# Kernel optimization log

Measured on AMD Instinct MI355X. Metric: run time of the kernel, lower is better.

## Reference

```python
import jax, jax.numpy as jnp
import numpy as np

N = 30000
E = 600000
IN = 64
HID = 128
EPS = 1e-5
HEADS_PER_LAYER = (4, 4, 1)


def _bn(x, g, b):
    # eval-mode BatchNorm: running_mean=0, running_var=1
    return x * (g / np.sqrt(1.0 + EPS)) + b


def _segment_softmax(e, dst, n):
    m = jax.ops.segment_max(e, dst, num_segments=n)
    ex = jnp.exp(e - m[dst])
    s = jax.ops.segment_sum(ex, dst, num_segments=n)
    return ex / (s[dst] + 1e-16)


def _gcn_conv(x, w, b, src, dst, norm, n):
    m = (x @ w)[src] * norm[:, None]            # [E+N, HID]
    return jax.ops.segment_sum(m, dst, num_segments=n) + b


def _gat_conv(x, w, a_src, a_dst, b, src, dst, n, heads):
    C = HID // heads
    xh = (x @ w).reshape(n, heads, C)
    asrc = (xh * a_src.reshape(heads, C)).sum(-1)   # [N, heads]
    adst = (xh * a_dst.reshape(heads, C)).sum(-1)
    e = jax.nn.leaky_relu(asrc[src] + adst[dst], 0.2)  # [E+N, heads]
    alpha = _segment_softmax(e, dst, n)
    out = jax.ops.segment_sum(xh[src] * alpha[:, :, None], dst, num_segments=n)
    return out.reshape(n, HID) + b


def _forward(x, gcn_in_w, gcn_in_b, gcn_res_w, gcn_res_b, gcn_w, gcn_b,
             gcn_bn_g, gcn_bn_b, gcn_c1w, gcn_c1b, gcn_c2w, gcn_c2b,
             gcn_c3w, gcn_c3b, gat_in_w, gat_in_b, gat_w, gat_asrc,
             gat_adst, gat_b, gat_bn_g, gat_bn_b, feat_imp, gat_c1w,
             gat_c1b, gat_cbn_g, gat_cbn_b, gat_c2w, gat_c2b, gat_c3w,
             gat_c3b, fin_w, fin_b, fin_bn_g, fin_bn_b, fin2_w, fin2_b,
             edge_index):
    n = x.shape[0]
    loop = jnp.arange(n, dtype=edge_index.dtype)
    src = jnp.concatenate([edge_index[0], loop])  # add self-loops
    dst = jnp.concatenate([edge_index[1], loop])
    # GCN symmetric normalization (with self-loops)
    deg = jax.ops.segment_sum(jnp.ones_like(dst, dtype=x.dtype), dst, num_segments=n)
    dis = jnp.where(deg > 0, jax.lax.rsqrt(jnp.maximum(deg, 1.0)), 0.0)
    norm = dis[src] * dis[dst]

    # ---- GCN branch (eval: dropout = identity, self-attn skipped since N>5000) ----
    xp = x @ gcn_in_w + gcn_in_b
    res = x @ gcn_res_w + gcn_res_b
    for i in range(3):
        xn = _gcn_conv(xp, gcn_w[i], gcn_b[i], src, dst, norm, n)
        xn = jax.nn.relu(_bn(xn, gcn_bn_g[i], gcn_bn_b[i]))
        if i % 2 == 1:
            xp = xn + res
            res = xp
        else:
            xp = xn
    h = jax.nn.relu(xp @ gcn_c1w + gcn_c1b)
    h = jax.nn.relu(h @ gcn_c2w + gcn_c2b)
    gcn_out = h @ gcn_c3w + gcn_c3b

    # ---- GAT branch ----
    xg = x @ gat_in_w + gat_in_b
    for i in range(3):
        xg = _gat_conv(xg, gat_w[i], gat_asrc[i], gat_adst[i], gat_b[i],
                       src, dst, n, HEADS_PER_LAYER[i])
        xg = jax.nn.elu(_bn(xg, gat_bn_g[i], gat_bn_b[i]))
    xg = xg * feat_imp
    h = jax.nn.relu(xg @ gat_c1w + gat_c1b)
    h = _bn(h, gat_cbn_g, gat_cbn_b)
    h = jax.nn.relu(h @ gat_c2w + gat_c2b)
    gat_out = h @ gat_c3w + gat_c3b

    # ---- fusion: N > 10000 -> weighted blend path ----
    fused = 0.6 * gcn_out + 0.4 * gat_out
    h = jax.nn.relu(fused @ fin_w + fin_b)
    h = _bn(h, fin_bn_g, fin_bn_b)
    return h @ fin2_w + fin2_b  # [N, 2]


def setup_inputs() -> dict:
    key = jax.random.key(0)
    ks = iter(jax.random.split(key, 64))

    def nrm(shape, scale=1.0):
        return jax.random.normal(next(ks), shape, dtype=jnp.float32) * scale

    s_in = 1.0 / np.sqrt(IN)
    s_h = 1.0 / np.sqrt(HID)
    inp = {}
    inp['x'] = nrm((N, IN))
    inp['edge_index'] = jax.random.randint(next(ks), (2, E), 0, N, dtype=jnp.int32)
    inp['gcn_in_w'] = nrm((IN, HID), s_in); inp['gcn_in_b'] = nrm((HID,), 0.01)
    inp['gcn_res_w'] = nrm((IN, HID), s_in); inp['gcn_res_b'] = nrm((HID,), 0.01)
    inp['gcn_w'] = nrm((3, HID, HID), s_h); inp['gcn_b'] = nrm((3, HID), 0.01)
    inp['gcn_bn_g'] = 1.0 + nrm((3, HID), 0.1); inp['gcn_bn_b'] = nrm((3, HID), 0.1)
    inp['gcn_c1w'] = nrm((HID, 64), s_h); inp['gcn_c1b'] = nrm((64,), 0.01)
    inp['gcn_c2w'] = nrm((64, 32), 0.125); inp['gcn_c2b'] = nrm((32,), 0.01)
    inp['gcn_c3w'] = nrm((32, HID), 0.18); inp['gcn_c3b'] = nrm((HID,), 0.01)
    inp['gat_in_w'] = nrm((IN, HID), s_in); inp['gat_in_b'] = nrm((HID,), 0.01)
    inp['gat_w'] = nrm((3, HID, HID), s_h)
    inp['gat_asrc'] = nrm((3, HID), s_h); inp['gat_adst'] = nrm((3, HID), s_h)
    inp['gat_b'] = nrm((3, HID), 0.01)
    inp['gat_bn_g'] = 1.0 + nrm((3, HID), 0.1); inp['gat_bn_b'] = nrm((3, HID), 0.1)
    inp['feat_imp'] = 1.0 + nrm((HID,), 0.1)
    inp['gat_c1w'] = nrm((HID, 64), s_h); inp['gat_c1b'] = nrm((64,), 0.01)
    inp['gat_cbn_g'] = 1.0 + nrm((64,), 0.1); inp['gat_cbn_b'] = nrm((64,), 0.1)
    inp['gat_c2w'] = nrm((64, 32), 0.125); inp['gat_c2b'] = nrm((32,), 0.01)
    inp['gat_c3w'] = nrm((32, HID), 0.18); inp['gat_c3b'] = nrm((HID,), 0.01)
    inp['fin_w'] = nrm((HID, 64), s_h); inp['fin_b'] = nrm((64,), 0.01)
    inp['fin_bn_g'] = 1.0 + nrm((64,), 0.1); inp['fin_bn_b'] = nrm((64,), 0.1)
    inp['fin2_w'] = nrm((64, 2), 0.125); inp['fin2_b'] = nrm((2,), 0.01)
    return inp


def reference(x, edge_index, gcn_in_w, gcn_in_b, gcn_res_w, gcn_res_b, gcn_w,
              gcn_b, gcn_bn_g, gcn_bn_b, gcn_c1w, gcn_c1b, gcn_c2w, gcn_c2b,
              gcn_c3w, gcn_c3b, gat_in_w, gat_in_b, gat_w, gat_asrc, gat_adst,
              gat_b, gat_bn_g, gat_bn_b, feat_imp, gat_c1w, gat_c1b, gat_cbn_g,
              gat_cbn_b, gat_c2w, gat_c2b, gat_c3w, gat_c3b, fin_w, fin_b,
              fin_bn_g, fin_bn_b, fin2_w, fin2_b):
    return _forward(x, gcn_in_w, gcn_in_b, gcn_res_w, gcn_res_b, gcn_w, gcn_b,
                    gcn_bn_g, gcn_bn_b, gcn_c1w, gcn_c1b, gcn_c2w, gcn_c2b,
                    gcn_c3w, gcn_c3b, gat_in_w, gat_in_b, gat_w, gat_asrc,
                    gat_adst, gat_b, gat_bn_g, gat_bn_b, feat_imp, gat_c1w,
                    gat_c1b, gat_cbn_g, gat_cbn_b, gat_c2w, gat_c2b, gat_c3w,
                    gat_c3b, fin_w, fin_b, fin_bn_g, fin_bn_b, fin2_w, fin2_b,
                    edge_index)
```

## Files before the change

kernel.cpp:

```cpp
#include <hip/hip_runtime.h>
#include <hip/hip_fp16.h>

#define RSQ_BN 0.9999950000374997f

typedef _Float16 f16x8 __attribute__((ext_vector_type(8)));
typedef float f32x4 __attribute__((ext_vector_type(4)));

__device__ __forceinline__ float leaky02(float x) { return x > 0.f ? x : 0.2f * x; }

__device__ __forceinline__ float4 ld4(const float* p) {
    return *reinterpret_cast<const float4*>(p);
}
__device__ __forceinline__ void st4(float* p, float4 v) {
    *reinterpret_cast<float4*>(p) = v;
}
__device__ __forceinline__ float4 h4f(uint2 u) {
    union { uint2 u; __half2 h[2]; } pk;
    pk.u = u;
    float2 lo = __half22float2(pk.h[0]);
    float2 hi = __half22float2(pk.h[1]);
    return make_float4(lo.x, lo.y, hi.x, hi.y);
}
__device__ __forceinline__ float4 f4z() { return make_float4(0.f, 0.f, 0.f, 0.f); }
__device__ __forceinline__ float4 f4bias(float4 v, float4 b) {
    return make_float4(v.x + b.x, v.y + b.y, v.z + b.z, v.w + b.w);
}
__device__ __forceinline__ float4 f4relu(float4 v) {
    return make_float4(fmaxf(v.x, 0.f), fmaxf(v.y, 0.f), fmaxf(v.z, 0.f), fmaxf(v.w, 0.f));
}
__device__ __forceinline__ float4 f4bn(float4 v, float4 g, float4 b) {
    return make_float4(v.x * g.x + b.x, v.y * g.y + b.y, v.z * g.z + b.z, v.w * g.w + b.w);
}
__device__ __forceinline__ float4 f4s(float4 v, float s) {
    return make_float4(v.x * s, v.y * s, v.z * s, v.w * s);
}


__global__ void zero_i32_k(int* __restrict__ p, int n) {
    int i = blockIdx.x * 256 + threadIdx.x;
    if (i < n) p[i] = 0;
}

__global__ void hist_k(const int* __restrict__ edst, int* __restrict__ cnt, int E, int EN) {
    int i = blockIdx.x * 256 + threadIdx.x;
    if (i >= EN) return;
    int d = (i < E) ? edst[i] : (i - E);
    atomicAdd(&cnt[d], 1);
}

__global__ __launch_bounds__(256)
void scanA_k(const int* __restrict__ cnt, int* __restrict__ rowptr,
             int* __restrict__ bsum, int n) {
    __shared__ int sh[256];
    int t = threadIdx.x;
    int i = blockIdx.x * 256 + t;
    int v = (i < n) ? cnt[i] : 0;
    sh[t] = v;
    __syncthreads();
#pragma unroll
    for (int off = 1; off < 256; off <<= 1) {
        int u = 0;
        if (t >= off) u = sh[t - off];
        __syncthreads();
        sh[t] += u;
        __syncthreads();
    }
    if (i < n) rowptr[i] = sh[t] - v;
    if (t == 255) bsum[blockIdx.x] = sh[255];
}

__global__ __launch_bounds__(256)
void scanB_k(int* __restrict__ bsum, int nb) {
    __shared__ int sh[256];
    int t = threadIdx.x;
    int v = (t < nb) ? bsum[t] : 0;
    sh[t] = v;
    __syncthreads();
#pragma unroll
    for (int off = 1; off < 256; off <<= 1) {
        int u = 0;
        if (t >= off) u = sh[t - off];
        __syncthreads();
        sh[t] += u;
        __syncthreads();
    }
    if (t < nb) bsum[t] = sh[t] - v;
}

__global__ __launch_bounds__(256)
void scanC_k(const int* __restrict__ cnt, const int* __restrict__ bsum,
             int* __restrict__ rowptr, int* __restrict__ cursor,
             float* __restrict__ dis, int n, int EN) {
    int i = blockIdx.x * 256 + threadIdx.x;
    if (i < n) {
        int r = rowptr[i] + bsum[blockIdx.x];
        rowptr[i] = r;
        cursor[i] = r;
        dis[i] = rsqrtf((float)cnt[i]);
    }
    if (i == 0) rowptr[n] = EN;
}

__global__ void scatter_k(const int* __restrict__ esrc, const int* __restrict__ edst,
                          int* __restrict__ cursor, int* __restrict__ colidx, int E, int EN) {
    int i = blockIdx.x * 256 + threadIdx.x;
    if (i >= EN) return;
    int s, d;
    if (i < E) { s = esrc[i]; d = edst[i]; }
    else       { s = i - E; d = s; }
    int pos = atomicAdd(&cursor[d], 1);
    colidx[pos] = s;
}


__global__ void wtx_all_k(const float* __restrict__ gcn_in_w, const float* __restrict__ gcn_res_w,
                          const float* __restrict__ gat_in_w,
                          const float* __restrict__ gcn_w, const float* __restrict__ gat_w,
                          const float* __restrict__ gcn_c1w, const float* __restrict__ gat_c1w,
                          const float* __restrict__ gcn_c3w, const float* __restrict__ gat_c3w,
                          const float* __restrict__ fin_w,
                          __half* __restrict__ WTin, __half* __restrict__ WTg,
                          __half* __restrict__ WTa, __half* __restrict__ WTc1,
                          __half* __restrict__ WTc3, __half* __restrict__ WTfin) {
    int idx = blockIdx.x * 256 + threadIdx.x;
    const float* src;
    __half* dst;
    int K, M, o;
    if (idx < 24576) {
        int mi = idx >> 13; o = idx & 8191;
        src = mi == 0 ? gcn_in_w : (mi == 1 ? gcn_res_w : gat_in_w);
        dst = WTin + mi * 8192; K = 64; M = 128;
    } else if (idx < 73728) {
        int r = idx - 24576; int mi = r >> 14; o = r & 16383;
        src = gcn_w + mi * 16384; dst = WTg + mi * 16384; K = 128; M = 128;
    } else if (idx < 122880) {
        int r = idx - 73728; int mi = r >> 14; o = r & 16383;
        src = gat_w + mi * 16384; dst = WTa + mi * 16384; K = 128; M = 128;
    } else if (idx < 139264) {
        int r = idx - 122880; int mi = r >> 13; o = r & 8191;
        src = mi ? gat_c1w : gcn_c1w; dst = WTc1 + mi * 8192; K = 128; M = 64;
    } else if (idx < 147456) {
        int r = idx - 139264; int mi = r >> 12; o = r & 4095;
        src = mi ? gat_c3w : gcn_c3w; dst = WTc3 + mi * 4096; K = 32; M = 128;
    } else if (idx < 155648) {
        o = idx - 147456; src = fin_w; dst = WTfin; K = 128; M = 64;
    } else return;
    int mcol = o / K, k = o - mcol * K;
    dst[o] = (__half)src[k * M + mcol];
}


#define FMA4R(A_, xv, w0, w1, w2, w3)                                  \
    A_.x += xv.x * w0.x + xv.y * w1.x + xv.z * w2.x + xv.w * w3.x;     \
    A_.y += xv.x * w0.y + xv.y * w1.y + xv.z * w2.y + xv.w * w3.y;     \
    A_.z += xv.x * w0.z + xv.y * w1.z + xv.z * w2.z + xv.w * w3.z;     \
    A_.w += xv.x * w0.w + xv.y * w1.w + xv.z * w2.w + xv.w * w3.w;

template <int K, int M>
__device__ __forceinline__ void gemm4(const float* __restrict__ Ws,
                                      const float* xa, const float* xb,
                                      const float* xc, const float* xd, int c,
                                      float4& A, float4& B, float4& C, float4& D) {
#pragma unroll 4
    for (int k = 0; k < K; k += 4) {
        float4 va = ld4(xa + k), vb = ld4(xb + k), vc = ld4(xc + k), vd = ld4(xd + k);
        const float* wp = Ws + k * M + c;
        float4 w0 = ld4(wp), w1 = ld4(wp + M), w2 = ld4(wp + 2 * M), w3 = ld4(wp + 3 * M);
        FMA4R(A, va, w0, w1, w2, w3)
        FMA4R(B, vb, w0, w1, w2, w3)
        FMA4R(C, vc, w0, w1, w2, w3)
        FMA4R(D, vd, w0, w1, w2, w3)
    }
}

template <int K, int M>
__global__ __launch_bounds__(256)
void tail2_k(const float* __restrict__ X0, const float* __restrict__ W0, const float* __restrict__ b0,
             float* __restrict__ Y0,
             const float* __restrict__ X1, const float* __restrict__ W1, const float* __restrict__ b1,
             float* __restrict__ Y1,
             int n, int gper, int do_relu) {
    constexpr int CG = M / 4, RPB = 256 / CG;
    bool s1 = blockIdx.x >= gper;
    int blk = s1 ? blockIdx.x - gper : blockIdx.x;
    const float* X = s1 ? X1 : X0;
    const float* W = s1 ? W1 : W0;
    const float* bi = s1 ? b1 : b0;
    float* Y = s1 ? Y1 : Y0;
    __shared__ float Ws[K * M];
    for (int i = threadIdx.x; i < K * M; i += 256) Ws[i] = W[i];
    __syncthreads();
    int cg = threadIdx.x % CG, r = threadIdx.x / CG, c = cg * 4;
    int ra = blk * (4 * RPB) + r, rb = ra + RPB, rc = ra + 2 * RPB, rd = ra + 3 * RPB;
    const float* xa = X + (size_t)(ra < n ? ra : 0) * K;
    const float* xb = X + (size_t)(rb < n ? rb : 0) * K;
    const float* xc = X + (size_t)(rc < n ? rc : 0) * K;
    const float* xd = X + (size_t)(rd < n ? rd : 0) * K;
    float4 A = f4z(), B = f4z(), C = f4z(), D = f4z();
    gemm4<K, M>(Ws, xa, xb, xc, xd, c, A, B, C, D);
    float4 bv = ld4(bi + c);
    A = f4bias(A, bv); B = f4bias(B, bv); C = f4bias(C, bv); D = f4bias(D, bv);
    if (do_relu) { A = f4relu(A); B = f4relu(B); C = f4relu(C); D = f4relu(D); }
    if (ra < n) st4(Y + (size_t)ra * M + c, A);
    if (rb < n) st4(Y + (size_t)rb * M + c, B);
    if (rc < n) st4(Y + (size_t)rc * M + c, C);
    if (rd < n) st4(Y + (size_t)rd * M + c, D);
}


__device__ __forceinline__ f16x8 mk_af(const float* xr, int kb) {
    float4 v0 = ld4(xr + kb), v1 = ld4(xr + kb + 4);
    f16x8 af;
    af[0] = (_Float16)v0.x; af[1] = (_Float16)v0.y;
    af[2] = (_Float16)v0.z; af[3] = (_Float16)v0.w;
    af[4] = (_Float16)v1.x; af[5] = (_Float16)v1.y;
    af[6] = (_Float16)v1.z; af[7] = (_Float16)v1.w;
    return af;
}

__global__ __launch_bounds__(256)
void mfma_lin3_k(const float* __restrict__ X, const __half* __restrict__ WTin,
                 const float* __restrict__ b0, float* __restrict__ Y0,
                 const float* __restrict__ b1, float* __restrict__ Y1,
                 const float* __restrict__ b2, float* __restrict__ Y2,
                 int n, int gper) {
    constexpr int K = 64, CT = 8;
    int set = blockIdx.x / gper, blk = blockIdx.x % gper;
    const __half* WT = WTin + (size_t)set * 8192;
    const float* bi = set == 0 ? b0 : (set == 1 ? b1 : b2);
    float* Y = set == 0 ? Y0 : (set == 1 ? Y1 : Y2);
    int wave = threadIdx.x >> 6, lane = threadIdx.x & 63;
    int m = lane & 15, quad = lane >> 4;
    int row0 = blk * 64 + wave * 16;
    int arow = min(row0 + m, n - 1);
    const float* xr = X + (size_t)arow * K;
    f32x4 acc[CT];
#pragma unroll
    for (int ct = 0; ct < CT; ++ct) acc[ct] = (f32x4){0.f, 0.f, 0.f, 0.f};
#pragma unroll
    for (int k32 = 0; k32 < K / 32; ++k32) {
        int kb = k32 * 32 + quad * 8;
        f16x8 af = mk_af(xr, kb);
#pragma unroll
        for (int ct = 0; ct < CT; ++ct) {
            f16x8 bf = *reinterpret_cast<const f16x8*>(WT + (size_t)(ct * 16 + m) * K + kb);
            acc[ct] = __builtin_amdgcn_mfma_f32_16x16x32_f16(af, bf, acc[ct], 0, 0, 0);
        }
    }
#pragma unroll
    for (int ct = 0; ct < CT; ++ct) {
        int col = ct * 16 + m;
        float cb = bi[col];
#pragma unroll
        for (int reg = 0; reg < 4; ++reg) {
            int row = row0 + quad * 4 + reg;
            if (row < n) Y[(size_t)row * 128 + col] = acc[ct][reg] + cb;
        }
    }
}

template <int K, int M>
__global__ __launch_bounds__(256)
void mfma_lin2_k(const float* __restrict__ X0, const __half* __restrict__ WT0,
                 const float* __restrict__ b0, const float* __restrict__ g0,
                 const float* __restrict__ bb0, float* __restrict__ Y0,
                 const float* __restrict__ X1, const __half* __restrict__ WT1,
                 const float* __restrict__ b1, const float* __restrict__ g1,
                 const float* __restrict__ bb1, float* __restrict__ Y1,
                 int n, int gper, int do_relu) {
    constexpr int CT = M / 16;
    bool s1 = blockIdx.x >= gper;
    int blk = s1 ? blockIdx.x - gper : blockIdx.x;
    const float* X = s1 ? X1 : X0;
    const __half* WT = s1 ? WT1 : WT0;
    const float* bi = s1 ? b1 : b0;
    const float* bg = s1 ? g1 : g0;
    const float* bb = s1 ? bb1 : bb0;
    float* Y = s1 ? Y1 : Y0;
    int wave = threadIdx.x >> 6, lane = threadIdx.x & 63;
    int m = lane & 15, quad = lane >> 4;
    int row0 = blk * 64 + wave * 16;
    int arow = min(row0 + m, n - 1);
    const float* xr = X + (size_t)arow * K;
    f32x4 acc[CT];
#pragma unroll
    for (int ct = 0; ct < CT; ++ct) acc[ct] = (f32x4){0.f, 0.f, 0.f, 0.f};
#pragma unroll
    for (int k32 = 0; k32 < K / 32; ++k32) {
        int kb = k32 * 32 + quad * 8;
        f16x8 af = mk_af(xr, kb);
#pragma unroll
        for (int ct = 0; ct < CT; ++ct) {
            f16x8 bf = *reinterpret_cast<const f16x8*>(WT + (size_t)(ct * 16 + m) * K + kb);
            acc[ct] = __builtin_amdgcn_mfma_f32_16x16x32_f16(af, bf, acc[ct], 0, 0, 0);
        }
    }
#pragma unroll
    for (int ct = 0; ct < CT; ++ct) {
        int col = ct * 16 + m;
        float cb = bi[col];
        float cg = bg ? bg[col] * RSQ_BN : 1.f;
        float cbb = bg ? bb[col] : 0.f;
#pragma unroll
        for (int reg = 0; reg < 4; ++reg) {
            int row = row0 + quad * 4 + reg;
            if (row < n) {
                float v = acc[ct][reg] + cb;
                if (do_relu) v = fmaxf(v, 0.f);
                if (bg) v = v * cg + cbb;
                Y[(size_t)row * M + col] = v;
            }
        }
    }
}

__global__ __launch_bounds__(256)
void mfma_linF_k(const float* __restrict__ XA, const float* __restrict__ XB,
                 const __half* __restrict__ WT, const float* __restrict__ bi,
                 const float* __restrict__ bg, const float* __restrict__ bb,
                 const float* __restrict__ w2, const float* __restrict__ b2,
                 float* __restrict__ out, int n) {
    constexpr int K = 128, M = 64, CT = 4;
    int wave = threadIdx.x >> 6, lane = threadIdx.x & 63;
    int m = lane & 15, quad = lane >> 4;
    int row0 = blockIdx.x * 64 + wave * 16;
    int arow = min(row0 + m, n - 1);
    const float* xra = XA + (size_t)arow * K;
    const float* xrb = XB + (size_t)arow * K;
    f32x4 acc[CT];
#pragma unroll
    for (int ct = 0; ct < CT; ++ct) acc[ct] = (f32x4){0.f, 0.f, 0.f, 0.f};
#pragma unroll
    for (int k32 = 0; k32 < K / 32; ++k32) {
        int kb = k32 * 32 + quad * 8;
        float4 a0 = ld4(xra + kb), a1 = ld4(xra + kb + 4);
        float4 u0 = ld4(xrb + kb), u1 = ld4(xrb + kb + 4);
        f16x8 af;
        af[0] = (_Float16)(0.6f * a0.x + 0.4f * u0.x);
        af[1] = (_Float16)(0.6f * a0.y + 0.4f * u0.y);
        af[2] = (_Float16)(0.6f * a0.z + 0.4f * u0.z);
        af[3] = (_Float16)(0.6f * a0.w + 0.4f * u0.w);
        af[4] = (_Float16)(0.6f * a1.x + 0.4f * u1.x);
        af[5] = (_Float16)(0.6f * a1.y + 0.4f * u1.y);
        af[6] = (_Float16)(0.6f * a1.z + 0.4f * u1.z);
        af[7] = (_Float16)(0.6f * a1.w + 0.4f * u1.w);
#pragma unroll
        for (int ct = 0; ct < CT; ++ct) {
            f16x8 bf = *reinterpret_cast<const f16x8*>(WT + (size_t)(ct * 16 + m) * K + kb);
            acc[ct] = __builtin_amdgcn_mfma_f32_16x16x32_f16(af, bf, acc[ct], 0, 0, 0);
        }
    }
    float p0[4] = {0.f, 0.f, 0.f, 0.f}, p1[4] = {0.f, 0.f, 0.f, 0.f};
#pragma unroll
    for (int ct = 0; ct < CT; ++ct) {
        int col = ct * 16 + m;
        float cb = bi[col];
        float cg = bg[col] * RSQ_BN;
        float cbb = bb[col];
        float w20 = w2[2 * col], w21 = w2[2 * col + 1];
#pragma unroll
        for (int reg = 0; reg < 4; ++reg) {
            float v = fmaxf(acc[ct][reg] + cb, 0.f) * cg + cbb;
            p0[reg] += v * w20;
            p1[reg] += v * w21;
        }
    }
    for (int off = 1; off < 16; off <<= 1) {
#pragma unroll
        for (int reg = 0; reg < 4; ++reg) {
            p0[reg] += __shfl_xor(p0[reg], off);
            p1[reg] += __shfl_xor(p1[reg], off);
        }
    }
    if (m == 0) {
#pragma unroll
        for (int reg = 0; reg < 4; ++reg) {
            int row = row0 + quad * 4 + reg;
            if (row < n) {
                out[row * 2] = p0[reg] + b2[0];
                out[row * 2 + 1] = p1[reg] + b2[1];
            }
        }
    }
}


__global__ __launch_bounds__(256)
void dual128_mfma_k(const float* __restrict__ Xg, const __half* __restrict__ WTg,
                    __half* __restrict__ Yg,
                    const float* __restrict__ Xa, const __half* __restrict__ WTa,
                    __half* __restrict__ Ya,
                    const float* __restrict__ dis,
                    const float* __restrict__ asrc, const float* __restrict__ adst,
                    float* __restrict__ avp, float* __restrict__ bvp,
                    int hh, int n, int gper) {
    bool gat = blockIdx.x >= gper;
    int blk = gat ? blockIdx.x - gper : blockIdx.x;
    const float* X = gat ? Xa : Xg;
    const __half* WT = gat ? WTa : WTg;
    __half* Y = gat ? Ya : Yg;
    int wave = threadIdx.x >> 6;
    int lane = threadIdx.x & 63;
    int m = lane & 15, quad = lane >> 4;
    int row0 = blk * 64 + wave * 16;
    int arow = min(row0 + m, n - 1);
    const float* xr = X + (size_t)arow * 128;
    f32x4 acc[8];
#pragma unroll
    for (int ct = 0; ct < 8; ++ct) acc[ct] = (f32x4){0.f, 0.f, 0.f, 0.f};
#pragma unroll
    for (int k32 = 0; k32 < 4; ++k32) {
        int kb = k32 * 32 + quad * 8;
        f16x8 af = mk_af(xr, kb);
#pragma unroll
        for (int ct = 0; ct < 8; ++ct) {
            f16x8 bf = *reinterpret_cast<const f16x8*>(WT + (size_t)(ct * 16 + m) * 128 + kb);
            acc[ct] = __builtin_amdgcn_mfma_f32_16x16x32_f16(af, bf, acc[ct], 0, 0, 0);
        }
    }
    if (!gat) {
#pragma unroll
        for (int reg = 0; reg < 4; ++reg) {
            int row = row0 + quad * 4 + reg;
            if (row < n) {
                float dv = dis[row];
#pragma unroll
                for (int ct = 0; ct < 8; ++ct)
                    Y[(size_t)row * 128 + ct * 16 + m] = (__half)(acc[ct][reg] * dv);
            }
        }
    } else {
        float cas[8], cad[8];
#pragma unroll
        for (int ct = 0; ct < 8; ++ct) {
            cas[ct] = asrc[ct * 16 + m];
            cad[ct] = adst[ct * 16 + m];
        }
        int ctph = 8 / hh;
#pragma unroll
        for (int reg = 0; reg < 4; ++reg) {
            int row = row0 + quad * 4 + reg;
            bool valid = row < n;
            if (valid) {
#pragma unroll
                for (int ct = 0; ct < 8; ++ct)
                    Y[(size_t)row * 128 + ct * 16 + m] = (__half)acc[ct][reg];
            }
            for (int h = 0; h < hh; ++h) {
                float sa = 0.f, sd = 0.f;
                for (int j = 0; j < ctph; ++j) {
                    int ct = h * ctph + j;
                    sa += acc[ct][reg] * cas[ct];
                    sd += acc[ct][reg] * cad[ct];
                }
                for (int off = 1; off < 16; off <<= 1) {
                    sa += __shfl_xor(sa, off);
                    sd += __shfl_xor(sd, off);
                }
                if (m == 0 && valid) {
                    avp[row * hh + h] = sa;
                    bvp[row * hh + h] = sd;
                }
            }
        }
    }
}


__global__ __launch_bounds__(256)
void fused_gather_k(const int* __restrict__ rowptr, const int* __restrict__ colidx,
                    const float* __restrict__ dis,
                    const __half* __restrict__ Tg, const float* __restrict__ gbias,
                    const float* __restrict__ gbng, const float* __restrict__ gbnb,
                    const float* __restrict__ res, float* __restrict__ Yg,
                    const __half* __restrict__ Ta, const float* __restrict__ avp,
                    const float* __restrict__ bvp, const float* __restrict__ abias,
                    const float* __restrict__ abng, const float* __restrict__ abnb,
                    const float* __restrict__ fimp, float* __restrict__ Ya,
                    int n, int hh, int log2C) {
    int idx = blockIdx.x * 256 + threadIdx.x;
    int i = idx >> 4;
    if (i >= n) return;
    int c = (idx & 15) * 8;
    int h = c >> log2C;
    float ad = bvp[i * hh + h];
    int p0 = rowptr[i], p1 = rowptr[i + 1];
    float4 glo = f4z(), ghi = f4z();
    float4 alo = f4z(), ahi = f4z();
    float m = -3.0e38f, s = 0.f;

#define GACC(qq)                                                                \
    {                                                                           \
        float4 t0 = h4f(make_uint2(qq.x, qq.y)), t1 = h4f(make_uint2(qq.z, qq.w)); \
        glo.x += t0.x; glo.y += t0.y; glo.z += t0.z; glo.w += t0.w;             \
        ghi.x += t1.x; ghi.y += t1.y; ghi.z += t1.z; ghi.w += t1.w;             \
    }
#define AACC(qq, ww)                                                            \
    {                                                                           \
        float4 t0 = h4f(make_uint2(qq.x, qq.y)), t1 = h4f(make_uint2(qq.z, qq.w)); \
        alo.x += t0.x * ww; alo.y += t0.y * ww; alo.z += t0.z * ww; alo.w += t0.w * ww; \
        ahi.x += t1.x * ww; ahi.y += t1.y * ww; ahi.z += t1.z * ww; ahi.w += t1.w * ww; \
    }

    int p = p0;
    int nfull = (p1 - p0) >> 2;
    int sx[4];
    if (nfull > 0) {
#pragma unroll
        for (int j = 0; j < 4; ++j) sx[j] = colidx[p + j];
    }
    for (int g = 0; g < nfull; ++g) {
        float e[4]; uint4 qg[4], qa[4];
#pragma unroll
        for (int j = 0; j < 4; ++j) e[j] = leaky02(avp[sx[j] * hh + h] + ad);
#pragma unroll
        for (int j = 0; j < 4; ++j)
            qg[j] = *reinterpret_cast<const uint4*>(Tg + (size_t)sx[j] * 128 + c);
#pragma unroll
        for (int j = 0; j < 4; ++j)
            qa[j] = *reinterpret_cast<const uint4*>(Ta + (size_t)sx[j] * 128 + c);
        int sn[4];
        int pn = p + 4;
        bool more = (g + 1) < nfull;
#pragma unroll
        for (int j = 0; j < 4; ++j) sn[j] = more ? colidx[pn + j] : 0;
#pragma unroll
        for (int j = 0; j < 4; ++j) GACC(qg[j])
        float mc = fmaxf(fmaxf(e[0], e[1]), fmaxf(e[2], e[3]));
        float mn = fmaxf(m, mc);
        float scale = expf(m - mn);
        alo = f4s(alo, scale);
        ahi = f4s(ahi, scale);
        float wsum = 0.f;
#pragma unroll
        for (int j = 0; j < 4; ++j) {
            float wj = expf(e[j] - mn);
            wsum += wj;
            AACC(qa[j], wj)
        }
        s = s * scale + wsum;
        m = mn;
        p = pn;
#pragma unroll
        for (int j = 0; j < 4; ++j) sx[j] = sn[j];
    }
    for (; p < p1; ++p) {
        int s0 = colidx[p];
        float e0 = leaky02(avp[s0 * hh + h] + ad);
        uint4 qg0 = *reinterpret_cast<const uint4*>(Tg + (size_t)s0 * 128 + c);
        uint4 qa0 = *reinterpret_cast<const uint4*>(Ta + (size_t)s0 * 128 + c);
        GACC(qg0)
        float mn = fmaxf(m, e0);
        float scale = expf(m - mn);
        float w0 = expf(e0 - mn);
        s = s * scale + w0;
        alo = f4s(alo, scale);
        ahi = f4s(ahi, scale);
        AACC(qa0, w0)
        m = mn;
    }

    {
        float di = dis[i];
        float4 b0 = ld4(gbias + c), b1 = ld4(gbias + c + 4);
        glo = make_float4(glo.x * di + b0.x, glo.y * di + b0.y, glo.z * di + b0.z, glo.w * di + b0.w);
        ghi = make_float4(ghi.x * di + b1.x, ghi.y * di + b1.y, ghi.z * di + b1.z, ghi.w * di + b1.w);
        float4 g0 = ld4(gbng + c), g1 = ld4(gbng + c + 4);
        g0 = f4s(g0, RSQ_BN); g1 = f4s(g1, RSQ_BN);
        float4 h0 = ld4(gbnb + c), h1 = ld4(gbnb + c + 4);
        glo = f4relu(f4bn(glo, g0, h0));
        ghi = f4relu(f4bn(ghi, g1, h1));
        if (res) {
            float4 r0 = ld4(res + (size_t)i * 128 + c), r1 = ld4(res + (size_t)i * 128 + c + 4);
            glo = f4bias(glo, r0); ghi = f4bias(ghi, r1);
        }
        st4(Yg + (size_t)i * 128 + c, glo);
        st4(Yg + (size_t)i * 128 + c + 4, ghi);
    }
    {
        float si = 1.f / (s + 1e-16f);
        float4 b0 = ld4(abias + c), b1 = ld4(abias + c + 4);
        alo = make_float4(alo.x * si + b0.x, alo.y * si + b0.y, alo.z * si + b0.z, alo.w * si + b0.w);
        ahi = make_float4(ahi.x * si + b1.x, ahi.y * si + b1.y, ahi.z * si + b1.z, ahi.w * si + b1.w);
        float4 g0 = ld4(abng + c), g1 = ld4(abng + c + 4);
        g0 = f4s(g0, RSQ_BN); g1 = f4s(g1, RSQ_BN);
        float4 h0 = ld4(abnb + c), h1 = ld4(abnb + c + 4);
        alo = f4bn(alo, g0, h0);
        ahi = f4bn(ahi, g1, h1);
        alo.x = alo.x > 0.f ? alo.x : expm1f(alo.x);
        alo.y = alo.y > 0.f ? alo.y : expm1f(alo.y);
        alo.z = alo.z > 0.f ? alo.z : expm1f(alo.z);
        alo.w = alo.w > 0.f ? alo.w : expm1f(alo.w);
        ahi.x = ahi.x > 0.f ? ahi.x : expm1f(ahi.x);
        ahi.y = ahi.y > 0.f ? ahi.y : expm1f(ahi.y);
        ahi.z = ahi.z > 0.f ? ahi.z : expm1f(ahi.z);
        ahi.w = ahi.w > 0.f ? ahi.w : expm1f(ahi.w);
        if (fimp) {
            float4 f0 = ld4(fimp + c), f1 = ld4(fimp + c + 4);
            alo = make_float4(alo.x * f0.x, alo.y * f0.y, alo.z * f0.z, alo.w * f0.w);
            ahi = make_float4(ahi.x * f1.x, ahi.y * f1.y, ahi.z * f1.z, ahi.w * f1.w);
        }
        st4(Ya + (size_t)i * 128 + c, alo);
        st4(Ya + (size_t)i * 128 + c + 4, ahi);
    }
#undef GACC
#undef AACC
}


static inline int cdiv(int a, int b) { return (a + b - 1) / b; }

extern "C" void kernel_launch(void* const* d_in, const int* in_sizes, int n_in,
                              void* d_out, int out_size, void* d_ws, size_t ws_size,
                              hipStream_t stream) {
    const float* x       = (const float*)d_in[0];
    const int*   ei      = (const int*)d_in[1];
    const float* gcn_in_w = (const float*)d_in[2];
    const float* gcn_in_b = (const float*)d_in[3];
    const float* gcn_res_w = (const float*)d_in[4];
    const float* gcn_res_b = (const float*)d_in[5];
    const float* gcn_w   = (const float*)d_in[6];
    const float* gcn_b   = (const float*)d_in[7];
    const float* gcn_bn_g = (const float*)d_in[8];
    const float* gcn_bn_b = (const float*)d_in[9];
    const float* gcn_c1w = (const float*)d_in[10];
    const float* gcn_c1b = (const float*)d_in[11];
    const float* gcn_c2w = (const float*)d_in[12];
    const float* gcn_c2b = (const float*)d_in[13];
    const float* gcn_c3w = (const float*)d_in[14];
    const float* gcn_c3b = (const float*)d_in[15];
    const float* gat_in_w = (const float*)d_in[16];
    const float* gat_in_b = (const float*)d_in[17];
    const float* gat_w   = (const float*)d_in[18];
    const float* gat_asrc = (const float*)d_in[19];
    const float* gat_adst = (const float*)d_in[20];
    const float* gat_b   = (const float*)d_in[21];
    const float* gat_bn_g = (const float*)d_in[22];
    const float* gat_bn_b = (const float*)d_in[23];
    const float* feat_imp = (const float*)d_in[24];
    const float* gat_c1w = (const float*)d_in[25];
    const float* gat_c1b = (const float*)d_in[26];
    const float* gat_cbn_g = (const float*)d_in[27];
    const float* gat_cbn_b = (const float*)d_in[28];
    const float* gat_c2w = (const float*)d_in[29];
    const float* gat_c2b = (const float*)d_in[30];
    const float* gat_c3w = (const float*)d_in[31];
    const float* gat_c3b = (const float*)d_in[32];
    const float* fin_w   = (const float*)d_in[33];
    const float* fin_b   = (const float*)d_in[34];
    const float* fin_bn_g = (const float*)d_in[35];
    const float* fin_bn_b = (const float*)d_in[36];
    const float* fin2_w  = (const float*)d_in[37];
    const float* fin2_b  = (const float*)d_in[38];

    const int N = in_sizes[0] / 64;
    const int E = in_sizes[1] / 2;
    const int EN = E + N;
    const int* esrc = ei;
    const int* edst = ei + E;

    char* wp = (char*)d_ws;
    auto alloc = [&](size_t bytes) -> void* {
        void* p = (void*)wp;
        wp += (bytes + 255) & ~(size_t)255;
        return p;
    };
    int* cnt    = (int*)alloc((size_t)N * 4);
    int* rowptr = (int*)alloc((size_t)(N + 1) * 4);
    int* cursor = (int*)alloc((size_t)N * 4);
    int* bsum   = (int*)alloc((size_t)256 * 4);
    int* colidx = (int*)alloc((size_t)EN * 4);
    float* dis  = (float*)alloc((size_t)N * 4);
    float* A    = (float*)alloc((size_t)N * 128 * 4);
    float* B    = (float*)alloc((size_t)N * 128 * 4);
    float* G    = (float*)alloc((size_t)N * 128 * 4);
    float* H    = (float*)alloc((size_t)N * 128 * 4);
    float* R    = (float*)alloc((size_t)N * 128 * 4);
    __half* Th1 = (__half*)alloc((size_t)N * 128 * 2);
    __half* Th2 = (__half*)alloc((size_t)N * 128 * 2);
    float* h2g  = (float*)alloc((size_t)N * 32 * 4);
    float* h2a  = (float*)alloc((size_t)N * 32 * 4);
    float* avv  = (float*)alloc((size_t)N * 4 * 4);
    float* bvv  = (float*)alloc((size_t)N * 4 * 4);
    __half* WTin = (__half*)alloc((size_t)3 * 8192 * 2);
    __half* WTg  = (__half*)alloc((size_t)3 * 16384 * 2);
    __half* WTa  = (__half*)alloc((size_t)3 * 16384 * 2);
    __half* WTc1 = (__half*)alloc((size_t)2 * 8192 * 2);
    __half* WTc3 = (__half*)alloc((size_t)2 * 4096 * 2);
    __half* WTfin = (__half*)alloc((size_t)8192 * 2);
    float* h1g = (float*)Th1;
    float* h1a = (float*)Th2;

    const int nScanB = cdiv(N, 256);
    zero_i32_k<<<cdiv(N, 256), 256, 0, stream>>>(cnt, N);
    hist_k<<<cdiv(EN, 256), 256, 0, stream>>>(edst, cnt, E, EN);
    scanA_k<<<nScanB, 256, 0, stream>>>(cnt, rowptr, bsum, N);
    scanB_k<<<1, 256, 0, stream>>>(bsum, nScanB);
    scanC_k<<<nScanB, 256, 0, stream>>>(cnt, bsum, rowptr, cursor, dis, N, EN);
    scatter_k<<<cdiv(EN, 256), 256, 0, stream>>>(esrc, edst, cursor, colidx, E, EN);
    wtx_all_k<<<608, 256, 0, stream>>>(gcn_in_w, gcn_res_w, gat_in_w, gcn_w, gat_w,
                                       gcn_c1w, gat_c1w, gcn_c3w, gat_c3w, fin_w,
                                       WTin, WTg, WTa, WTc1, WTc3, WTfin);

    const int g64r  = cdiv(N, 64);
    const int g128r = cdiv(N, 128);
    const int gG    = cdiv(N, 16);

    mfma_lin3_k<<<3 * g64r, 256, 0, stream>>>(x, WTin, gcn_in_b, A, gcn_res_b, R,
                                              gat_in_b, G, N, g64r);

    const int heads_arr[3] = {4, 4, 1};
    float* gcur = A; float* gnxt = B;
    float* acur = G; float* anxt = H;
    for (int i = 0; i < 3; ++i) {
        int hh = heads_arr[i];
        int log2C = (hh == 4) ? 5 : 7;
        dual128_mfma_k<<<2 * g64r, 256, 0, stream>>>(gcur, WTg + (size_t)i * 16384, Th1,
                                                     acur, WTa + (size_t)i * 16384, Th2, dis,
                                                     gat_asrc + i * 128, gat_adst + i * 128,
                                                     avv, bvv, hh, N, g64r);
        fused_gather_k<<<gG, 256, 0, stream>>>(rowptr, colidx, dis,
                                               Th1, gcn_b + i * 128, gcn_bn_g + i * 128,
                                               gcn_bn_b + i * 128, (i == 1) ? R : nullptr, gnxt,
                                               Th2, avv, bvv, gat_b + i * 128,
                                               gat_bn_g + i * 128, gat_bn_b + i * 128,
                                               (i == 2) ? feat_imp : nullptr, anxt,
                                               N, hh, log2C);
        float* t = gcur; gcur = gnxt; gnxt = t;
        t = acur; acur = anxt; anxt = t;
    }

    mfma_lin2_k<128, 64><<<2 * g64r, 256, 0, stream>>>(
        gcur, WTc1, gcn_c1b, nullptr, nullptr, h1g,
        acur, WTc1 + 8192, gat_c1b, gat_cbn_g, gat_cbn_b, h1a, N, g64r, 1);
    tail2_k<64, 32><<<2 * g128r, 256, 0, stream>>>(
        h1g, gcn_c2w, gcn_c2b, h2g,
        h1a, gat_c2w, gat_c2b, h2a, N, g128r, 1);
    mfma_lin2_k<32, 128><<<2 * g64r, 256, 0, stream>>>(
        h2g, WTc3, gcn_c3b, nullptr, nullptr, A,
        h2a, WTc3 + 4096, gat_c3b, nullptr, nullptr, G, N, g64r, 0);

    mfma_linF_k<<<g64r, 256, 0, stream>>>(A, G, WTfin, fin_b, fin_bn_g, fin_bn_b,
                                          fin2_w, fin2_b, (float*)d_out, N);
}
```

Before: 509.1 us.

## Sort nodes by degree to balance work in fused gather kernel

Adds a counting sort of nodes by in-degree (histogram, single-block scan, scatter into a permutation array). The fused GCN/GAT gather kernel then processes nodes in degree-sorted order via perm, so that each wavefront handles nodes with similar edge counts and divergence or imbalance inside a wave is reduced. This costs three extra small kernels plus a zeroing launch, and it makes row access and output writes non-contiguous, which can hurt locality.

```diff
diff --git a/kernel.cpp b/kernel.cpp
--- a/kernel.cpp
+++ b/kernel.cpp
@@ -110,6 +110,41 @@
     else       { s = i - E; d = s; }
     int pos = atomicAdd(&cursor[d], 1);
     colidx[pos] = s;
+}
+
+
+__global__ void deghist_k(const int* __restrict__ cnt, int* __restrict__ dh, int n) {
+    int i = blockIdx.x * 256 + threadIdx.x;
+    if (i < n) atomicAdd(&dh[min(cnt[i], 511)], 1);
+}
+
+__global__ __launch_bounds__(256)
+void degscan_k(int* __restrict__ dh) {
+    __shared__ int sh[512];
+    int t = threadIdx.x;
+    sh[t] = dh[t];
+    sh[t + 256] = dh[t + 256];
+    __syncthreads();
+#pragma unroll
+    for (int off = 1; off < 512; off <<= 1) {
+        int v0 = (t >= off) ? sh[t - off] : 0;
+        int v1 = (t + 256 >= off) ? sh[t + 256 - off] : 0;
+        __syncthreads();
+        sh[t] += v0;
+        sh[t + 256] += v1;
+        __syncthreads();
+    }
+    dh[t] = t ? sh[t - 1] : 0;
+    dh[t + 256] = sh[t + 255];
+}
+
+__global__ void degscatter_k(const int* __restrict__ cnt, int* __restrict__ dh,
+                             int* __restrict__ perm, int n) {
+    int i = blockIdx.x * 256 + threadIdx.x;
+    if (i < n) {
+        int pos = atomicAdd(&dh[min(cnt[i], 511)], 1);
+        perm[pos] = i;
+    }
 }
 
 
@@ -469,7 +504,7 @@
 
 __global__ __launch_bounds__(256)
 void fused_gather_k(const int* __restrict__ rowptr, const int* __restrict__ colidx,
-                    const float* __restrict__ dis,
+                    const int* __restrict__ perm, const float* __restrict__ dis,
                     const __half* __restrict__ Tg, const float* __restrict__ gbias,
                     const float* __restrict__ gbng, const float* __restrict__ gbnb,
                     const float* __restrict__ res, float* __restrict__ Yg,
@@ -479,8 +514,9 @@
                     const float* __restrict__ fimp, float* __restrict__ Ya,
                     int n, int hh, int log2C) {
     int idx = blockIdx.x * 256 + threadIdx.x;
-    int i = idx >> 4;
-    if (i >= n) return;
+    int ni = idx >> 4;
+    if (ni >= n) return;
+    int i = perm[ni];
     int c = (idx & 15) * 8;
     int h = c >> log2C;
     float ad = bvp[i * hh + h];
@@ -670,6 +706,8 @@
     int* cursor = (int*)alloc((size_t)N * 4);
     int* bsum   = (int*)alloc((size_t)256 * 4);
     int* colidx = (int*)alloc((size_t)EN * 4);
+    int* dh     = (int*)alloc((size_t)512 * 4);
+    int* perm   = (int*)alloc((size_t)N * 4);
     float* dis  = (float*)alloc((size_t)N * 4);
     float* A    = (float*)alloc((size_t)N * 128 * 4);
     float* B    = (float*)alloc((size_t)N * 128 * 4);
@@ -693,11 +731,15 @@
 
     const int nScanB = cdiv(N, 256);
     zero_i32_k<<<cdiv(N, 256), 256, 0, stream>>>(cnt, N);
+    zero_i32_k<<<2, 256, 0, stream>>>(dh, 512);
     hist_k<<<cdiv(EN, 256), 256, 0, stream>>>(edst, cnt, E, EN);
     scanA_k<<<nScanB, 256, 0, stream>>>(cnt, rowptr, bsum, N);
     scanB_k<<<1, 256, 0, stream>>>(bsum, nScanB);
     scanC_k<<<nScanB, 256, 0, stream>>>(cnt, bsum, rowptr, cursor, dis, N, EN);
     scatter_k<<<cdiv(EN, 256), 256, 0, stream>>>(esrc, edst, cursor, colidx, E, EN);
+    deghist_k<<<nScanB, 256, 0, stream>>>(cnt, dh, N);
+    degscan_k<<<1, 256, 0, stream>>>(dh);
+    degscatter_k<<<nScanB, 256, 0, stream>>>(cnt, dh, perm, N);
     wtx_all_k<<<608, 256, 0, stream>>>(gcn_in_w, gcn_res_w, gat_in_w, gcn_w, gat_w,
                                        gcn_c1w, gat_c1w, gcn_c3w, gat_c3w, fin_w,
                                        WTin, WTg, WTa, WTc1, WTc3, WTfin);
@@ -719,7 +761,7 @@
                                                      acur, WTa + (size_t)i * 16384, Th2, dis,
                                                      gat_asrc + i * 128, gat_adst + i * 128,
                                                      avv, bvv, hh, N, g64r);
-        fused_gather_k<<<gG, 256, 0, stream>>>(rowptr, colidx, dis,
+        fused_gather_k<<<gG, 256, 0, stream>>>(rowptr, colidx, perm, dis,
                                                Th1, gcn_b + i * 128, gcn_bn_g + i * 128,
                                                gcn_bn_b + i * 128, (i == 1) ? R : nullptr, gnxt,
                                                Th2, avv, bvv, gat_b + i * 128,
```

New measurement: 681.2 us. +33.8%, slower.
